# Kernel tuning notes

Hardware: AMD Instinct MI355X
Metric: run time of the kernel (lower is better)

Reference implementation:

```python
import jax, jax.numpy as jnp
import numpy as np

B, N, T, C64 = 32, 512, 24, 64


def setup_inputs() -> dict:
    key = jax.random.key(0)
    ks = jax.random.split(key, 32)
    s = 0.05
    rn = lambda k, shape: jax.random.normal(k, shape, jnp.float32) * s
    # Chebyshev polynomials of a symmetric 'scaled Laplacian' with spectral radius ~1
    rng = np.random.default_rng(0)
    A = rng.standard_normal((N, N)).astype(np.float32)
    L = (A + A.T) * (0.5 / np.sqrt(N))
    T0 = np.eye(N, dtype=np.float32)
    T1 = L
    T2 = 2.0 * (L @ L) - T0
    cheb = jnp.asarray(np.stack([T0, T1, T2]))  # (K,N,N)
    return dict(
        x=jax.random.normal(ks[0], (B, N, 1, T), jnp.float32),
        y=jax.random.normal(ks[1], (B, T, 151), jnp.float32),
        tl_w=rn(ks[2], (C64 * T, 151 * T)), tl_b=rn(ks[3], (C64 * T,)),
        u0_w=rn(ks[4], (C64 * T, T)), u0_b=rn(ks[5], (C64 * T,)),
        u1a=rn(ks[6], (N,)), u2a=rn(ks[7], (C64, N)), u3a=rn(ks[8], (C64,)),
        be_a=rn(ks[9], (1, T, T)), ve_a=rn(ks[10], (T, T)),
        u1b=rn(ks[11], (N,)), u2b=rn(ks[12], (C64, N)), u3b=rn(ks[13], (C64,)),
        be_b=rn(ks[14], (1, T, T)), ve_b=rn(ks[15], (T, T)),
        sw1=rn(ks[16], (T,)), sw2=rn(ks[17], (1, T)), sw3=rn(ks[18], (1,)),
        s_bs=rn(ks[19], (1, N, N)), s_vs=rn(ks[20], (N, N)),
        cheb=cheb, theta=rn(ks[21], (3, 1, C64)),
        l1_w=rn(ks[22], (C64 * T, C64 * T)), l1_b=rn(ks[23], (C64 * T,)),
        res_w=rn(ks[24], (C64,)), res_b=rn(ks[25], (C64,)),
        ln_g=jnp.ones((C64,), jnp.float32), ln_b=jnp.zeros((C64,), jnp.float32),
    )


def reference(x, y, tl_w, tl_b, u0_w, u0_b, u1a, u2a, u3a, be_a, ve_a,
              u1b, u2b, u3b, be_b, ve_b, sw1, sw2, sw3, s_bs, s_vs,
              cheb, theta, l1_w, l1_b, res_w, res_b, ln_g, ln_b):
    b, n, fin, t = x.shape
    # datetime embedding: Linear(151*T -> 64*T), reshaped to (B,T,64)
    dt = (y.reshape(b, -1) @ tl_w.T + tl_b).reshape(b, t, C64)

    def temporal_att(x64, u1, u2, u3, be, ve):
        # x64: (B,N,64,T); add dt broadcast over vertices
        x1 = x64 + jnp.transpose(dt, (0, 2, 1))[:, None]          # (B,N,64,T)
        lhs = jnp.einsum('bnft,n,fm->btm', x1, u1, u2)            # (B,T,N)
        rhs = jnp.einsum('f,bnft->bnt', u3, x1)                   # (B,N,T)
        prod = jnp.einsum('btn,bns->bts', lhs, rhs)               # (B,T,T)
        E = jnp.einsum('ts,bsr->btr', ve, jax.nn.sigmoid(prod + be))
        return jax.nn.softmax(E, axis=1)

    # TAt with F_in == 1: U0 (1x1 Conv1d over T channels) expands to 64 features
    xin = jnp.transpose(x.reshape(b, n, t), (0, 2, 1))            # (B,T,N)
    x0 = jnp.einsum('ot,btn->bon', u0_w, xin) + u0_b[None, :, None]  # (B,64T,N)
    x64 = jnp.transpose(x0, (0, 2, 1)).reshape(b, n, C64, t)
    E1 = temporal_att(x64, u1a, u2a, u3a, be_a, ve_a)             # (B,T,T)

    # apply temporal attention: (B,N*F,T) @ (B,T,T)
    x_tat = jnp.einsum('bnft,bts->bnfs', x, E1)                   # (B,N,1,T)

    # spatial attention
    lhs = jnp.einsum('bnft,t,fm->bnm', x_tat, sw1, sw2)           # (B,N,T)
    rhs = jnp.einsum('f,bnft->btn', sw3, x_tat)                   # (B,T,N)
    prod = jnp.einsum('bnt,btm->bnm', lhs, rhs)                   # (B,N,N)
    S = jnp.einsum('nm,bmk->bnk', s_vs, jax.nn.sigmoid(prod + s_bs))
    S = jax.nn.softmax(S, axis=1)                                 # (B,N,N)

    # K-order Chebyshev graph conv with spatial attention (vectorized over T)
    g = jnp.zeros((b, n, theta.shape[-1], t), x.dtype)
    for k in range(cheb.shape[0]):
        At = jnp.transpose(cheb[k][None] * S, (0, 2, 1))          # (B,N,N)
        tmp = jnp.einsum('bij,bjft->bift', At, x)                 # (B,N,1,T)
        g = g + jnp.einsum('bift,fo->biot', tmp, theta[k])
    g = jax.nn.relu(g)                                            # (B,N,64,T)

    # second temporal attention (F=64 path, no U0)
    E2 = temporal_att(g, u1b, u2b, u3b, be_b, ve_b)
    g2 = jnp.einsum('bnfs,bst->bnft', g, E2)                      # (B,N,64,T)

    # linear1 over flattened (64*T), then raw reshape to (B,64,N,T)
    tlin = g2.reshape(b, n, -1) @ l1_w.T + l1_b                   # (B,N,64T)
    tco = tlin.reshape(b, C64, n, t)

    # residual 1x1 conv: in_channels=1 -> 64
    res = x[:, :, 0, :][:, None] * res_w[None, :, None, None] + res_b[None, :, None, None]

    z = jax.nn.relu(res + tco)                                    # (B,64,N,T)
    z = jnp.transpose(z, (0, 3, 2, 1))                            # (B,T,N,64)
    mu = jnp.mean(z, axis=-1, keepdims=True)
    var = jnp.var(z, axis=-1, keepdims=True)
    z = (z - mu) / jnp.sqrt(var + 1e-5) * ln_g + ln_b
    return jnp.transpose(z, (0, 2, 3, 1))                         # (B,N,64,T)
```

## Files before the change

kernel.cpp:

```cpp
#include <hip/hip_runtime.h>
#include <hip/hip_bf16.h>
#include <math.h>

#define BB 32
#define NN 512
#define TT 24
#define CC 64
#define CT 1536
#define YD 3624
#define YP 3648

typedef __attribute__((ext_vector_type(4))) float f32x4;
typedef __attribute__((ext_vector_type(8))) short bf16x8;

static __device__ __forceinline__ short f2bf(float f){
  union { float f; unsigned u; } v; v.f = f;
  unsigned r = (v.u + 0x7FFF + ((v.u >> 16) & 1)) >> 16;
  return (short)r;
}
static __device__ __forceinline__ float bf2f(short s){
  union { unsigned u; float f; } v; v.u = ((unsigned)(unsigned short)s) << 16;
  return v.f;
}

__global__ void k_prep0(const float* __restrict__ u0_w, const float* __restrict__ u0_b,
                        const float* __restrict__ u1a, const float* __restrict__ u3a,
                        const float* __restrict__ u1b,
                        float* __restrict__ w0u3, float* __restrict__ b0u3, float* __restrict__ sums){
  int tid = threadIdx.x;
  if (tid < 576){
    int tp = tid / TT, t = tid % TT;
    float acc = 0.f;
    for (int f = 0; f < CC; ++f) acc += u3a[f] * u0_w[(f*TT + tp)*TT + t];
    w0u3[tid] = acc;
  }
  if (tid < TT){
    float acc = 0.f;
    for (int f = 0; f < CC; ++f) acc += u3a[f] * u0_b[f*TT + tid];
    b0u3[tid] = acc;
  }
  if (tid == 0){ float s = 0.f; for (int n = 0; n < NN; ++n) s += u1a[n]; sums[0] = s; }
  if (tid == 1){ float s = 0.f; for (int n = 0; n < NN; ++n) s += u1b[n]; sums[1] = s; }
}

__global__ __launch_bounds__(256) void k_pre(const float* __restrict__ s_vs, const float* __restrict__ y,
                    const float* __restrict__ tl_w, const float* __restrict__ cheb,
                    const float* __restrict__ x, const float* __restrict__ l1_w,
                    const float* __restrict__ s_bs,
                    __hip_bfloat16* __restrict__ svB, __hip_bfloat16* __restrict__ yB,
                    __hip_bfloat16* __restrict__ WB, short* __restrict__ chT,
                    short* __restrict__ xTb, __hip_bfloat16* __restrict__ Wb,
                    float* __restrict__ sbT){
  __shared__ float shm[512*25];
  int bb = blockIdx.x, tid = threadIdx.x;
  if (bb < 256){
    int i = (bb*256 + tid)*4;
    float4 v = *(const float4*)(s_vs + i);
    svB[i+0] = __float2bfloat16(v.x);
    svB[i+1] = __float2bfloat16(v.y);
    svB[i+2] = __float2bfloat16(v.z);
    svB[i+3] = __float2bfloat16(v.w);
  } else if (bb < 313){
    int gid = (bb - 256)*256 + tid;
    int r = gid / (YP/8), c8 = (gid % (YP/8))*8;
    if (r < 32){
      bf16x8 o;
      if (c8 < YD){
        float4 a = *(const float4*)(y + (size_t)r*YD + c8);
        float4 b = *(const float4*)(y + (size_t)r*YD + c8 + 4);
        o[0]=f2bf(a.x); o[1]=f2bf(a.y); o[2]=f2bf(a.z); o[3]=f2bf(a.w);
        o[4]=f2bf(b.x); o[5]=f2bf(b.y); o[6]=f2bf(b.z); o[7]=f2bf(b.w);
      } else {
        for (int j = 0; j < 8; ++j) o[j] = 0;
      }
      *(bf16x8*)((short*)yB + (size_t)r*YP + c8) = o;
    }
  } else if (bb < 3049){
    int gid = (bb - 313)*256 + tid;
    int r = gid / (YP/8), c8 = (gid % (YP/8))*8;
    if (r < 1536){
      bf16x8 o;
      if (c8 < YD){
        float4 a = *(const float4*)(tl_w + (size_t)r*YD + c8);
        float4 b = *(const float4*)(tl_w + (size_t)r*YD + c8 + 4);
        o[0]=f2bf(a.x); o[1]=f2bf(a.y); o[2]=f2bf(a.z); o[3]=f2bf(a.w);
        o[4]=f2bf(b.x); o[5]=f2bf(b.y); o[6]=f2bf(b.z); o[7]=f2bf(b.w);
      } else {
        for (int j = 0; j < 8; ++j) o[j] = 0;
      }
      *(bf16x8*)((short*)WB + (size_t)r*YP + c8) = o;
    }
  } else if (bb < 3817){
    int q = bb - 3049;
    int jt = q & 15, it = (q >> 4) & 15, k = q >> 8;
    float (*ts)[33] = (float(*)[33])shm;
    int c = tid & 31, r8 = tid >> 5;
    #pragma unroll
    for (int p = 0; p < 4; ++p){
      int r = p*8 + r8;
      ts[r][c] = cheb[((size_t)k*NN + jt*32 + r)*NN + it*32 + c];
    }
    __syncthreads();
    #pragma unroll
    for (int p = 0; p < 4; ++p){
      int r = p*8 + r8;
      chT[((size_t)k*NN + it*32 + r)*NN + jt*32 + c] = f2bf(ts[c][r]);
    }
  } else if (bb < 3849){
    int b = bb - 3817;
    for (int idx = tid; idx < NN*TT; idx += 256){
      int j = idx / TT, t = idx % TT;
      shm[j*25 + t] = x[(size_t)b*NN*TT + idx];
    }
    __syncthreads();
    for (int u = tid; u < 32*64; u += 256){
      int t = u >> 6, j8 = (u & 63)*8;
      bf16x8 o;
      if (t < TT){
        #pragma unroll
        for (int e = 0; e < 8; ++e) o[e] = f2bf(shm[(j8 + e)*25 + t]);
      } else {
        #pragma unroll
        for (int e = 0; e < 8; ++e) o[e] = 0;
      }
      *(bf16x8*)(xTb + ((size_t)b*32 + t)*NN + j8) = o;
    }
  } else if (bb < 6153){
    int i = ((bb - 3849)*256 + tid)*4;
    float4 v = *(const float4*)(l1_w + i);
    Wb[i+0] = __float2bfloat16(v.x);
    Wb[i+1] = __float2bfloat16(v.y);
    Wb[i+2] = __float2bfloat16(v.z);
    Wb[i+3] = __float2bfloat16(v.w);
  } else {
    int q = bb - 6153;
    int mt = q & 15, kt = q >> 4;
    float (*ts)[33] = (float(*)[33])shm;
    int c = tid & 31, r8 = tid >> 5;
    #pragma unroll
    for (int p = 0; p < 4; ++p){
      int r = p*8 + r8;
      ts[r][c] = s_bs[(size_t)(mt*32 + r)*NN + kt*32 + c];
    }
    __syncthreads();
    #pragma unroll
    for (int p = 0; p < 4; ++p){
      int r = p*8 + r8;
      sbT[(size_t)(kt*32 + r)*NN + mt*32 + c] = ts[c][r];
    }
  }
}

__global__ __launch_bounds__(256) void k_dtgemm(const __hip_bfloat16* __restrict__ yB,
                       const __hip_bfloat16* __restrict__ WB, float* __restrict__ pdt){
  __shared__ __align__(16) short lA[32*32];
  __shared__ __align__(16) short lB[256*32];
  int nt = blockIdx.x, ks = blockIdx.y;
  int o0 = nt*256;
  int tid = threadIdx.x;
  int w = tid >> 6, l = tid & 63;
  int lrow = l & 15, lk = l >> 4;
  f32x4 acc[2][4];
  #pragma unroll
  for (int m = 0; m < 2; ++m)
    #pragma unroll
    for (int n = 0; n < 4; ++n) acc[m][n] = (f32x4){0.f,0.f,0.f,0.f};
  for (int step = 0; step < 6; ++step){
    int k0 = (ks*6 + step)*32;
    #pragma unroll
    for (int p = 0; p < 4; ++p){
      int c = p*4 + w;
      int off = c*512 + l*8;
      int row = off >> 5, col = off & 31;
      __builtin_amdgcn_global_load_lds(
        (const __attribute__((address_space(1))) void*)((const short*)WB + (size_t)(o0 + row)*YP + k0 + col),
        (__attribute__((address_space(3))) void*)(lB + c*512), 16, 0, 0);
    }
    if (w < 2){
      int off = w*512 + l*8;
      int row = off >> 5, col = off & 31;
      __builtin_amdgcn_global_load_lds(
        (const __attribute__((address_space(1))) void*)((const short*)yB + (size_t)row*YP + k0 + col),
        (__attribute__((address_space(3))) void*)(lA + w*512), 16, 0, 0);
    }
    __syncthreads();
    bf16x8 a[2], bv[4];
    #pragma unroll
    for (int m = 0; m < 2; ++m) a[m] = *(const bf16x8*)(lA + (m*16 + lrow)*32 + lk*8);
    #pragma unroll
    for (int n = 0; n < 4; ++n) bv[n] = *(const bf16x8*)(lB + (w*64 + n*16 + lrow)*32 + lk*8);
    #pragma unroll
    for (int m = 0; m < 2; ++m)
      #pragma unroll
      for (int n = 0; n < 4; ++n)
        acc[m][n] = __builtin_amdgcn_mfma_f32_16x16x32_bf16(a[m], bv[n], acc[m][n], 0, 0, 0);
    __syncthreads();
  }
  #pragma unroll
  for (int m = 0; m < 2; ++m){
    #pragma unroll
    for (int n = 0; n < 4; ++n){
      int o = o0 + w*64 + n*16 + lrow;
      #pragma unroll
      for (int j = 0; j < 4; ++j){
        int b = m*16 + lk*4 + j;
        pdt[((size_t)(ks*32 + b))*CT + o] = acc[m][n][j];
      }
    }
  }
}

__global__ void k_small(const float* __restrict__ x, const float* __restrict__ pdt,
                        const float* __restrict__ tl_b,
                        const float* __restrict__ u0_w, const float* __restrict__ u0_b,
                        const float* __restrict__ u1a, const float* __restrict__ u3a,
                        const float* __restrict__ u3b, const float* __restrict__ sums,
                        float* __restrict__ dt,
                        float* __restrict__ w1a, float* __restrict__ du3a, float* __restrict__ du3b){
  __shared__ float xu_s[TT], u1a_s[NN], dt_s[CT];
  int b = blockIdx.x, tid = threadIdx.x;
  for (int o = tid; o < CT; o += 256){
    float acc = tl_b[o];
    #pragma unroll
    for (int ks = 0; ks < 19; ++ks) acc += pdt[((size_t)(ks*32 + b))*CT + o];
    dt_s[o] = acc;
    dt[b*CT + o] = acc;
  }
  for (int i = tid; i < NN; i += 256) u1a_s[i] = u1a[i];
  __syncthreads();
  int wv = tid >> 6, ln = tid & 63;
  for (int t = wv; t < TT; t += 4){
    float acc = 0.f;
    for (int n = ln; n < NN; n += 64) acc += u1a_s[n]*x[(size_t)(b*NN + n)*TT + t];
    for (int off = 32; off; off >>= 1) acc += __shfl_down(acc, off);
    if (ln == 0) xu_s[t] = acc;
  }
  if (tid < TT){
    float a = 0.f, c = 0.f;
    for (int f = 0; f < CC; ++f){
      float d = dt_s[tid*CC + f];
      a += u3a[f]*d; c += u3b[f]*d;
    }
    du3a[b*TT + tid] = a;
    du3b[b*TT + tid] = c;
  }
  __syncthreads();
  float S1 = sums[0];
  for (int idx = tid; idx < CC*TT; idx += 256){
    int f = idx / TT, tp = idx % TT;
    float acc = 0.f;
    const float* wrow = u0_w + (f*TT + tp)*TT;
    for (int t = 0; t < TT; ++t) acc += wrow[t]*xu_s[t];
    w1a[b*CC*TT + idx] = acc + S1*(u0_b[f*TT + tp] + dt_s[tp*CC + f]);
  }
}

__global__ __launch_bounds__(384) void k_rhs1(const float* __restrict__ x, const float* __restrict__ w0u3,
                      const float* __restrict__ b0u3, const float* __restrict__ du3a,
                      float* __restrict__ rhs1){
  __shared__ float xs[16*TT], w0_s[576], bd_s[TT];
  int b = blockIdx.y, n0 = blockIdx.x*16, tid = threadIdx.x;
  for (int i = tid; i < 576; i += 384) w0_s[i] = w0u3[i];
  if (tid < TT) bd_s[tid] = b0u3[tid] + du3a[b*TT + tid];
  xs[tid] = x[(size_t)(b*NN + n0)*TT + tid];
  __syncthreads();
  int nn = tid / TT, tp = tid % TT;
  float acc = bd_s[tp];
  const float* wr = w0_s + tp*TT;
  const float* xr = xs + nn*TT;
  for (int t = 0; t < TT; ++t) acc += wr[t]*xr[t];
  rhs1[(size_t)b*NN*TT + (n0 + nn)*TT + tp] = acc;
}

__global__ __launch_bounds__(576) void k_prod(const float* __restrict__ u2, const float* __restrict__ w1,
                      const float* __restrict__ rhs, float* __restrict__ pprod){
  __shared__ float u2s[64][65], w1s[CC*TT], lh[TT][64], rh[64][TT];
  int ns = blockIdx.x, b = blockIdx.y;
  int n0 = ns*64, tid = threadIdx.x;
  for (int i = tid; i < 4096; i += 576){ int f = i >> 6, n = i & 63; u2s[f][n] = u2[f*NN + n0 + n]; }
  for (int i = tid; i < CC*TT; i += 576) w1s[i] = w1[b*CC*TT + i];
  for (int i = tid; i < 1536; i += 576) ((float*)rh)[i] = rhs[(size_t)b*NN*TT + n0*TT + i];
  __syncthreads();
  for (int idx = tid; idx < 1536; idx += 576){
    int t = idx >> 6, n = idx & 63;
    float acc = 0.f;
    #pragma unroll 8
    for (int f = 0; f < CC; ++f) acc += u2s[f][n]*w1s[f*TT + t];
    lh[t][n] = acc;
  }
  __syncthreads();
  int t = tid / TT, s = tid % TT;
  float acc = 0.f;
  #pragma unroll 4
  for (int n = 0; n < 64; ++n) acc += lh[t][n]*rh[n][s];
  pprod[((size_t)(b*8 + ns))*576 + tid] = acc;
}

__global__ void k_att_post2(const float* __restrict__ pprod, const float* __restrict__ ve,
                            const float* __restrict__ be, float* __restrict__ E){
  __shared__ float sig_s[TT*TT], E_s[TT*TT];
  int b = blockIdx.x, tid = threadIdx.x;
  float acc = 0.f;
  #pragma unroll
  for (int p = 0; p < 8; ++p) acc += pprod[((size_t)(b*8 + p))*576 + tid];
  sig_s[tid] = 1.f/(1.f + expf(-(acc + be[tid])));
  __syncthreads();
  {
    int t = tid / TT, r = tid % TT;
    float a = 0.f;
    for (int s = 0; s < TT; ++s) a += ve[t*TT + s]*sig_s[s*TT + r];
    E_s[tid] = a;
  }
  __syncthreads();
  if (tid < TT){
    int r = tid;
    float mx = -1e30f;
    for (int t = 0; t < TT; ++t) mx = fmaxf(mx, E_s[t*TT + r]);
    float sum = 0.f;
    for (int t = 0; t < TT; ++t) sum += expf(E_s[t*TT + r] - mx);
    float inv = 1.f/sum;
    for (int t = 0; t < TT; ++t) E[(size_t)b*TT*TT + t*TT + r] = expf(E_s[t*TT + r] - mx)*inv;
  }
}

__global__ void k_xtat(const float* __restrict__ x, const float* __restrict__ E1,
                       const float* __restrict__ sw1, const float* __restrict__ sw2,
                       const float* __restrict__ sw3,
                       float* __restrict__ lx, float* __restrict__ r2){
  __shared__ float E_s[TT*TT], sw1_s[TT], sw2_s[TT];
  int b = blockIdx.x >> 1, half = blockIdx.x & 1, tid = threadIdx.x;
  for (int i = tid; i < 576; i += 256) E_s[i] = E1[(size_t)b*576 + i];
  if (tid < TT){ sw1_s[tid] = sw1[tid]; sw2_s[tid] = sw2[tid]; }
  __syncthreads();
  int n = half*256 + tid;
  float xr[TT];
  const float* xp = x + (size_t)(b*NN + n)*TT;
  for (int t = 0; t < TT; ++t) xr[t] = xp[t];
  float l = 0.f, r = 0.f;
  for (int s = 0; s < TT; ++s){
    float acc = 0.f;
    for (int t = 0; t < TT; ++t) acc += xr[t]*E_s[t*TT + s];
    l += acc*sw1_s[s];
    r += acc*sw2_s[s];
  }
  lx[b*NN + n] = l;
  r2[b*NN + n] = r*sw3[0];
}

__global__ __launch_bounds__(256) void k_sig(const float* __restrict__ lx, const float* __restrict__ r2,
                     const float* __restrict__ sbT, short* __restrict__ Qb){
  int b = blockIdx.y;
  int k = blockIdx.x*4 + (threadIdx.x >> 6);
  int m8 = (threadIdx.x & 63)*8;
  float r2k = r2[b*NN + k];
  const float* lxb = lx + b*NN;
  float4 l0 = *(const float4*)(lxb + m8);
  float4 l1 = *(const float4*)(lxb + m8 + 4);
  const float* sb = sbT + (size_t)k*NN + m8;
  float4 s0 = *(const float4*)(sb);
  float4 s1 = *(const float4*)(sb + 4);
  bf16x8 o;
  o[0] = f2bf(1.f/(1.f + __expf(-(l0.x*r2k + s0.x))));
  o[1] = f2bf(1.f/(1.f + __expf(-(l0.y*r2k + s0.y))));
  o[2] = f2bf(1.f/(1.f + __expf(-(l0.z*r2k + s0.z))));
  o[3] = f2bf(1.f/(1.f + __expf(-(l0.w*r2k + s0.w))));
  o[4] = f2bf(1.f/(1.f + __expf(-(l1.x*r2k + s1.x))));
  o[5] = f2bf(1.f/(1.f + __expf(-(l1.y*r2k + s1.y))));
  o[6] = f2bf(1.f/(1.f + __expf(-(l1.z*r2k + s1.z))));
  o[7] = f2bf(1.f/(1.f + __expf(-(l1.w*r2k + s1.w))));
  *(bf16x8*)(Qb + ((size_t)b*NN + k)*NN + m8) = o;
}

__global__ __launch_bounds__(256) void k_S0(const __hip_bfloat16* __restrict__ svB,
                    const short* __restrict__ Qb, float* __restrict__ ST){
  __shared__ __align__(16) short lA[128*32];
  __shared__ __align__(16) short lB[128*32];
  int kt = blockIdx.x, nt = blockIdx.y, b = blockIdx.z;
  int n0 = nt*128, k0 = kt*128;
  int tid = threadIdx.x;
  int w = tid >> 6, l = tid & 63;
  int wr = w >> 1, wc = w & 1;
  int lrow = l & 15, lk = l >> 4;
  f32x4 acc[4][4];
  #pragma unroll
  for (int m = 0; m < 4; ++m)
    #pragma unroll
    for (int n = 0; n < 4; ++n) acc[m][n] = (f32x4){0.f,0.f,0.f,0.f};
  for (int m0 = 0; m0 < NN; m0 += 32){
    #pragma unroll
    for (int p = 0; p < 2; ++p){
      int c = p*4 + w;
      int off = c*512 + l*8;
      int row = off >> 5, col = off & 31;
      __builtin_amdgcn_global_load_lds(
        (const __attribute__((address_space(1))) void*)(svB + (size_t)(n0 + row)*NN + m0 + col),
        (__attribute__((address_space(3))) void*)(lA + c*512), 16, 0, 0);
      __builtin_amdgcn_global_load_lds(
        (const __attribute__((address_space(1))) void*)(Qb + ((size_t)b*NN + k0 + row)*NN + m0 + col),
        (__attribute__((address_space(3))) void*)(lB + c*512), 16, 0, 0);
    }
    __syncthreads();
    bf16x8 a[4], bv[4];
    #pragma unroll
    for (int m = 0; m < 4; ++m) a[m] = *(const bf16x8*)(lA + (wr*64 + m*16 + lrow)*32 + lk*8);
    #pragma unroll
    for (int n = 0; n < 4; ++n) bv[n] = *(const bf16x8*)(lB + (wc*64 + n*16 + lrow)*32 + lk*8);
    #pragma unroll
    for (int m = 0; m < 4; ++m)
      #pragma unroll
      for (int n = 0; n < 4; ++n)
        acc[m][n] = __builtin_amdgcn_mfma_f32_16x16x32_bf16(a[m], bv[n], acc[m][n], 0, 0, 0);
    __syncthreads();
  }
  #pragma unroll
  for (int m = 0; m < 4; ++m){
    #pragma unroll
    for (int n = 0; n < 4; ++n){
      int col = k0 + wc*64 + n*16 + lrow;
      int row = n0 + wr*64 + m*16 + lk*4;
      float4 v; v.x = acc[m][n][0]; v.y = acc[m][n][1]; v.z = acc[m][n][2]; v.w = acc[m][n][3];
      *(float4*)(ST + (size_t)b*NN*NN + (size_t)col*NN + row) = v;
    }
  }
}

__global__ __launch_bounds__(256) void k_expS(const float* __restrict__ ST, short* __restrict__ P,
                      float* __restrict__ invZ){
  int b = blockIdx.y;
  int row = blockIdx.x*4 + (threadIdx.x >> 6);
  int l = threadIdx.x & 63;
  const float* R = ST + (size_t)b*NN*NN + (size_t)row*NN;
  float4 v0 = *(const float4*)(R + l*8);
  float4 v1 = *(const float4*)(R + l*8 + 4);
  float mx = fmaxf(fmaxf(fmaxf(v0.x,v0.y),fmaxf(v0.z,v0.w)),
                   fmaxf(fmaxf(v1.x,v1.y),fmaxf(v1.z,v1.w)));
  for (int off = 32; off; off >>= 1) mx = fmaxf(mx, __shfl_xor(mx, off));
  v0.x = __expf(v0.x-mx); v0.y = __expf(v0.y-mx); v0.z = __expf(v0.z-mx); v0.w = __expf(v0.w-mx);
  v1.x = __expf(v1.x-mx); v1.y = __expf(v1.y-mx); v1.z = __expf(v1.z-mx); v1.w = __expf(v1.w-mx);
  float s = v0.x+v0.y+v0.z+v0.w+v1.x+v1.y+v1.z+v1.w;
  for (int off = 32; off; off >>= 1) s += __shfl_xor(s, off);
  bf16x8 o;
  o[0]=f2bf(v0.x); o[1]=f2bf(v0.y); o[2]=f2bf(v0.z); o[3]=f2bf(v0.w);
  o[4]=f2bf(v1.x); o[5]=f2bf(v1.y); o[6]=f2bf(v1.z); o[7]=f2bf(v1.w);
  *(bf16x8*)(P + ((size_t)b*NN + row)*NN + l*8) = o;
  if (l == 0) invZ[b*NN + row] = 1.f/s;
}

__global__ __launch_bounds__(256) void k_tmpG(const short* __restrict__ P, const short* __restrict__ chebT,
                      const short* __restrict__ xT, const float* __restrict__ invZ,
                      float* __restrict__ tmp){
  __shared__ __align__(16) short lP[128*32];
  __shared__ __align__(16) short lC[128*32];
  __shared__ __align__(16) short lX[32*32];
  __shared__ float iz_s[128];
  int it = blockIdx.x, kc = blockIdx.y, b = blockIdx.z;
  int i0 = it*128;
  int tid = threadIdx.x;
  int w = tid >> 6, l = tid & 63;
  int lrow = l & 15, lk = l >> 4;
  if (tid < 128) iz_s[tid] = invZ[b*NN + i0 + tid];
  f32x4 acc[2][2];
  #pragma unroll
  for (int m = 0; m < 2; ++m)
    #pragma unroll
    for (int n = 0; n < 2; ++n) acc[m][n] = (f32x4){0.f,0.f,0.f,0.f};
  for (int ks = 0; ks < 16; ++ks){
    int k0 = ks*32;
    #pragma unroll
    for (int p = 0; p < 2; ++p){
      int c = p*4 + w;
      int off = c*512 + l*8;
      int row = off >> 5, col = off & 31;
      __builtin_amdgcn_global_load_lds(
        (const __attribute__((address_space(1))) void*)(P + ((size_t)b*NN + i0 + row)*NN + k0 + col),
        (__attribute__((address_space(3))) void*)(lP + c*512), 16, 0, 0);
      __builtin_amdgcn_global_load_lds(
        (const __attribute__((address_space(1))) void*)(chebT + ((size_t)kc*NN + i0 + row)*NN + k0 + col),
        (__attribute__((address_space(3))) void*)(lC + c*512), 16, 0, 0);
    }
    if (w < 2){
      int off = w*512 + l*8;
      int row = off >> 5, col = off & 31;
      __builtin_amdgcn_global_load_lds(
        (const __attribute__((address_space(1))) void*)(xT + ((size_t)b*32 + row)*NN + k0 + col),
        (__attribute__((address_space(3))) void*)(lX + w*512), 16, 0, 0);
    }
    __syncthreads();
    bf16x8 a[2], bv[2];
    #pragma unroll
    for (int m = 0; m < 2; ++m){
      int r = w*32 + m*16 + lrow;
      bf16x8 pp = *(const bf16x8*)(lP + r*32 + lk*8);
      bf16x8 cc = *(const bf16x8*)(lC + r*32 + lk*8);
      bf16x8 af;
      #pragma unroll
      for (int e = 0; e < 8; ++e) af[e] = f2bf(bf2f(pp[e])*bf2f(cc[e]));
      a[m] = af;
    }
    #pragma unroll
    for (int n = 0; n < 2; ++n) bv[n] = *(const bf16x8*)(lX + (n*16 + lrow)*32 + lk*8);
    #pragma unroll
    for (int m = 0; m < 2; ++m)
      #pragma unroll
      for (int n = 0; n < 2; ++n)
        acc[m][n] = __builtin_amdgcn_mfma_f32_16x16x32_bf16(a[m], bv[n], acc[m][n], 0, 0, 0);
    __syncthreads();
  }
  #pragma unroll
  for (int m = 0; m < 2; ++m){
    #pragma unroll
    for (int n = 0; n < 2; ++n){
      int t = n*16 + lrow;
      if (t < TT){
        #pragma unroll
        for (int j = 0; j < 4; ++j){
          int ir = w*32 + m*16 + lk*4 + j;
          tmp[((size_t)(kc*BB + b)*NN + i0 + ir)*TT + t] = acc[m][n][j]*iz_s[ir];
        }
      }
    }
  }
}

__global__ __launch_bounds__(384) void k_gsum(const float* __restrict__ tmp, const float* __restrict__ theta,
                      const float* __restrict__ u1b, const float* __restrict__ u3b,
                      const float* __restrict__ du3b,
                      float* __restrict__ rhsg, float* __restrict__ pw1g){
  __shared__ float A0[16*TT], A1[16*TT], A2[16*TT], th_s[192], u3_s[CC], u1_s[16], du_s[TT];
  int nt = blockIdx.x, b = blockIdx.y;
  int n0 = nt*16, tid = threadIdx.x;
  for (int i = tid; i < 192; i += 384) th_s[i] = theta[i];
  if (tid < CC) u3_s[tid] = u3b[tid];
  if (tid < 16) u1_s[tid] = u1b[n0 + tid];
  if (tid < TT) du_s[tid] = du3b[b*TT + tid];
  A0[tid] = tmp[((size_t)(0*BB + b)*NN + n0)*TT + tid];
  A1[tid] = tmp[((size_t)(1*BB + b)*NN + n0)*TT + tid];
  A2[tid] = tmp[((size_t)(2*BB + b)*NN + n0)*TT + tid];
  __syncthreads();
  {
    int nn = tid / TT, t = tid % TT;
    float a0 = A0[nn*TT + t], a1 = A1[nn*TT + t], a2 = A2[nn*TT + t];
    float acc = du_s[t];
    #pragma unroll 8
    for (int f = 0; f < CC; ++f){
      float v = th_s[f]*a0 + th_s[64 + f]*a1 + th_s[128 + f]*a2;
      acc += u3_s[f]*fmaxf(v, 0.f);
    }
    rhsg[(size_t)b*NN*TT + (n0 + nn)*TT + t] = acc;
  }
  #pragma unroll
  for (int p = 0; p < 4; ++p){
    int o = tid + p*384;
    int f = o / TT, t = o % TT;
    float t0 = th_s[f], t1 = th_s[64 + f], t2 = th_s[128 + f];
    float acc = 0.f;
    #pragma unroll
    for (int m = 0; m < 16; ++m){
      float v = t0*A0[m*TT + t] + t1*A1[m*TT + t] + t2*A2[m*TT + t];
      acc += u1_s[m]*fmaxf(v, 0.f);
    }
    pw1g[((size_t)(b*32 + nt))*CC*TT + o] = acc;
  }
}

__global__ void k_w1g_red(const float* __restrict__ pw1g, const float* __restrict__ dt,
                          const float* __restrict__ sums, float* __restrict__ w1g){
  int b = blockIdx.x, tid = threadIdx.x;
  float S2 = sums[1];
  for (int o = tid; o < CC*TT; o += 256){
    int f = o / TT, t = o % TT;
    float acc = 0.f;
    for (int nt = 0; nt < 32; ++nt) acc += pw1g[((size_t)(b*32 + nt))*CC*TT + o];
    w1g[b*CC*TT + o] = acc + S2*dt[b*CT + t*CC + f];
  }
}

__global__ void k_g2(const float* __restrict__ tmp, const float* __restrict__ E2,
                     const float* __restrict__ theta, __hip_bfloat16* __restrict__ g2){
  __shared__ float E_s[TT*TT], th_s[192], tr[3*4*TT], g_s[4*CT];
  int b = blockIdx.y, n0 = blockIdx.x*4, tid = threadIdx.x;
  for (int i = tid; i < 576; i += 256) E_s[i] = E2[(size_t)b*576 + i];
  for (int i = tid; i < 192; i += 256) th_s[i] = theta[i];
  for (int i = tid; i < 288; i += 256){
    int k = i / 96, rem = i % 96, nn = rem / TT, s = rem % TT;
    tr[i] = tmp[((size_t)(k*BB + b)*NN + n0 + nn)*TT + s];
  }
  __syncthreads();
  for (int idx = tid; idx < 4*CT; idx += 256){
    int nn = idx / CT, rem = idx % CT, f = rem / TT, s = rem % TT;
    float v = th_s[f]*tr[nn*TT + s] + th_s[64 + f]*tr[96 + nn*TT + s] + th_s[128 + f]*tr[192 + nn*TT + s];
    g_s[idx] = fmaxf(v, 0.f);
  }
  __syncthreads();
  for (int idx = tid; idx < 4*CT; idx += 256){
    int nn = idx / CT, rem = idx % CT, f = rem / TT, t = rem % TT;
    float acc = 0.f;
    const float* gr = g_s + nn*CT + f*TT;
    for (int s = 0; s < TT; ++s) acc += gr[s]*E_s[s*TT + t];
    g2[(size_t)(b*NN + n0 + nn)*CT + rem] = __float2bfloat16(acc);
  }
}

__global__ __launch_bounds__(256) void k_gemm_bf16(const __hip_bfloat16* __restrict__ A,
                      const __hip_bfloat16* __restrict__ W,
                      const float* __restrict__ bias, __hip_bfloat16* __restrict__ Cout){
  int bid = blockIdx.x;
  int nb = (bid & 7)*192 + (bid >> 3);
  int o0 = (nb % 12)*128, i0 = (nb / 12)*128;
  __shared__ __align__(16) short lA[128*64];
  __shared__ __align__(16) short lB[128*64];
  int tid = threadIdx.x;
  int w = tid >> 6, l = tid & 63;
  int wr = w >> 1, wc = w & 1;
  int lrow = l & 15, lk = l >> 4;
  int srow = l >> 3;
  int scol = ((l & 7) ^ srow)*8;
  int swz = (lrow & 7) << 3;
  f32x4 acc[4][4];
  #pragma unroll
  for (int m = 0; m < 4; ++m)
    #pragma unroll
    for (int n = 0; n < 4; ++n) acc[m][n] = (f32x4){0.f,0.f,0.f,0.f};
  for (int k0 = 0; k0 < CT; k0 += 64){
    #pragma unroll
    for (int p = 0; p < 4; ++p){
      int c = p*4 + w;
      __builtin_amdgcn_global_load_lds(
        (const __attribute__((address_space(1))) void*)(A + (size_t)(i0 + c*8 + srow)*CT + k0 + scol),
        (__attribute__((address_space(3))) void*)(lA + c*512), 16, 0, 0);
      __builtin_amdgcn_global_load_lds(
        (const __attribute__((address_space(1))) void*)(W + (size_t)(o0 + c*8 + srow)*CT + k0 + scol),
        (__attribute__((address_space(3))) void*)(lB + c*512), 16, 0, 0);
    }
    __syncthreads();
    #pragma unroll
    for (int h = 0; h < 2; ++h){
      bf16x8 a[4], bv[4];
      #pragma unroll
      for (int m = 0; m < 4; ++m){
        int row = wr*64 + m*16 + lrow;
        a[m] = *(const bf16x8*)(lA + row*64 + ((h*32 + lk*8) ^ swz));
      }
      #pragma unroll
      for (int n = 0; n < 4; ++n){
        int row = wc*64 + n*16 + lrow;
        bv[n] = *(const bf16x8*)(lB + row*64 + ((h*32 + lk*8) ^ swz));
      }
      #pragma unroll
      for (int m = 0; m < 4; ++m)
        #pragma unroll
        for (int n = 0; n < 4; ++n)
          acc[m][n] = __builtin_amdgcn_mfma_f32_16x16x32_bf16(a[m], bv[n], acc[m][n], 0, 0, 0);
    }
    __syncthreads();
  }
  #pragma unroll
  for (int m = 0; m < 4; ++m){
    #pragma unroll
    for (int n = 0; n < 4; ++n){
      int o = o0 + wc*64 + n*16 + lrow;
      float bo = bias[o];
      #pragma unroll
      for (int j = 0; j < 4; ++j){
        int i = i0 + wr*64 + m*16 + lk*4 + j;
        Cout[(size_t)i*CT + o] = __float2bfloat16(acc[m][n][j] + bo);
      }
    }
  }
}

__global__ __launch_bounds__(128) void k_final(const __hip_bfloat16* __restrict__ tlin, const float* __restrict__ x,
                      const float* __restrict__ res_w, const float* __restrict__ res_b,
                      const float* __restrict__ ln_g, const float* __restrict__ ln_b,
                      float* __restrict__ out){
  __shared__ float Ls[64][132];
  __shared__ float rw_s[64], rb_s[64], lg_s[64], lb_s[64];
  int ot = blockIdx.x, dlt = blockIdx.y, b = blockIdx.z;
  int o0 = ot*128, tid = threadIdx.x;
  if (tid < 64){ rw_s[tid]=res_w[tid]; rb_s[tid]=res_b[tid]; lg_s[tid]=ln_g[tid]; lb_s[tid]=ln_b[tid]; }
  const __hip_bfloat16* tb = tlin + (size_t)b*NN*CT;
  #pragma unroll 4
  for (int c = 0; c < 64; ++c)
    Ls[c][tid] = __bfloat162float(tb[(size_t)(c*8 + dlt)*CT + o0 + tid]);
  __syncthreads();
  int p = dlt*CT + o0 + tid;
  int np = p / TT, tp = p % TT;
  float xv = x[(size_t)(b*NN + np)*TT + tp];
  float z[CC];
  float sum = 0.f, sq = 0.f;
  #pragma unroll
  for (int c = 0; c < CC; ++c){
    float v = Ls[c][tid] + xv*rw_s[c] + rb_s[c];
    v = fmaxf(v, 0.f);
    z[c] = v; sum += v; sq += v*v;
  }
  float mu = sum*(1.f/64.f);
  float var = sq*(1.f/64.f) - mu*mu;
  float rstd = rsqrtf(var + 1e-5f);
  float* ob = out + (size_t)(b*NN + np)*CC*TT + tp;
  #pragma unroll
  for (int c = 0; c < CC; ++c)
    ob[c*TT] = (z[c] - mu)*rstd*lg_s[c] + lb_s[c];
}

extern "C" void kernel_launch(void* const* d_in, const int* in_sizes, int n_in,
                              void* d_out, int out_size, void* d_ws, size_t ws_size,
                              hipStream_t stream){
  const float* x    = (const float*)d_in[0];
  const float* y    = (const float*)d_in[1];
  const float* tl_w = (const float*)d_in[2];
  const float* tl_b = (const float*)d_in[3];
  const float* u0_w = (const float*)d_in[4];
  const float* u0_b = (const float*)d_in[5];
  const float* u1a  = (const float*)d_in[6];
  const float* u2a  = (const float*)d_in[7];
  const float* u3a  = (const float*)d_in[8];
  const float* be_a = (const float*)d_in[9];
  const float* ve_a = (const float*)d_in[10];
  const float* u1b  = (const float*)d_in[11];
  const float* u2b  = (const float*)d_in[12];
  const float* u3b  = (const float*)d_in[13];
  const float* be_b = (const float*)d_in[14];
  const float* ve_b = (const float*)d_in[15];
  const float* sw1  = (const float*)d_in[16];
  const float* sw2  = (const float*)d_in[17];
  const float* sw3  = (const float*)d_in[18];
  const float* s_bs = (const float*)d_in[19];
  const float* s_vs = (const float*)d_in[20];
  const float* cheb = (const float*)d_in[21];
  const float* theta= (const float*)d_in[22];
  const float* l1_w = (const float*)d_in[23];
  const float* l1_b = (const float*)d_in[24];
  const float* res_w= (const float*)d_in[25];
  const float* res_b= (const float*)d_in[26];
  const float* ln_g = (const float*)d_in[27];
  const float* ln_b = (const float*)d_in[28];
  float* out = (float*)d_out;
  float* ws  = (float*)d_ws;

  float* dt   = ws;
  float* E    = dt   + 49152;
  float* lxp  = E    + 18432;
  float* r2p  = lxp  + 16384;
  float* w0u3 = r2p  + 16384;
  float* b0u3 = w0u3 + 640;
  float* sums = b0u3 + 64;
  float* du3a = sums + 64;
  float* du3b = du3a + 768;
  float* w1a  = du3b + 768;
  float* w1g  = w1a  + 49152;
  float* lhs1 = w1g  + 49152;
  float* rhs1 = lhs1 + 393216;
  float* lhsg = rhs1 + 393216;
  float* rhsg = lhsg + 393216;
  float* svBf = rhsg + 393216;
  float* ppr  = svBf + 131072;
  float* tmp  = ppr  + 147456;
  float* big  = tmp  + 1179648;
  float* ST   = big;
  float* pw1g = big;
  __hip_bfloat16* tlin = (__hip_bfloat16*)big;
  __hip_bfloat16* WB = (__hip_bfloat16*)big;
  __hip_bfloat16* yB = (__hip_bfloat16*)(big + 2801664);
  float* pdt = big + 2801664 + 58368;
  short* Pb  = (short*)(big + 8388608);
  short* xTb = (short*)(big + 12582912);
  float* iZ  = big + 12582912 + 262144;
  short* chT = (short*)(big + 12582912 + 262144 + 16384);
  __hip_bfloat16* Wb = (__hip_bfloat16*)(big + 13254656);
  short* Qb  = (short*)(big + 14434304);
  float* sbT = big + 18628608;
  __hip_bfloat16* svB = (__hip_bfloat16*)svBf;
  __hip_bfloat16* g2b = (__hip_bfloat16*)d_out;

  k_prep0<<<dim3(1), dim3(576), 0, stream>>>(u0_w, u0_b, u1a, u3a, u1b, w0u3, b0u3, sums);
  k_pre<<<dim3(6409), dim3(256), 0, stream>>>(s_vs, y, tl_w, cheb, x, l1_w, s_bs, svB, yB, WB, chT, xTb, Wb, sbT);
  k_dtgemm<<<dim3(6, 19), dim3(256), 0, stream>>>(yB, WB, pdt);
  k_small<<<dim3(32), dim3(256), 0, stream>>>(x, pdt, tl_b, u0_w, u0_b, u1a, u3a, u3b, sums, dt, w1a, du3a, du3b);
  k_rhs1<<<dim3(32, 32), dim3(384), 0, stream>>>(x, w0u3, b0u3, du3a, rhs1);
  k_prod<<<dim3(8, 32), dim3(576), 0, stream>>>(u2a, w1a, rhs1, ppr);
  k_att_post2<<<dim3(32), dim3(576), 0, stream>>>(ppr, ve_a, be_a, E);
  k_xtat<<<dim3(64), dim3(256), 0, stream>>>(x, E, sw1, sw2, sw3, lxp, r2p);
  k_sig<<<dim3(128, 32), dim3(256), 0, stream>>>(lxp, r2p, sbT, Qb);
  k_S0<<<dim3(4, 4, 32), dim3(256), 0, stream>>>(svB, Qb, ST);
  k_expS<<<dim3(128, 32), dim3(256), 0, stream>>>(ST, Pb, iZ);
  k_tmpG<<<dim3(4, 3, 32), dim3(256), 0, stream>>>(Pb, chT, xTb, iZ, tmp);
  k_gsum<<<dim3(32, 32), dim3(384), 0, stream>>>(tmp, theta, u1b, u3b, du3b, rhsg, pw1g);
  k_w1g_red<<<dim3(32), dim3(256), 0, stream>>>(pw1g, dt, sums, w1g);
  k_prod<<<dim3(8, 32), dim3(576), 0, stream>>>(u2b, w1g, rhsg, ppr);
  k_att_post2<<<dim3(32), dim3(576), 0, stream>>>(ppr, ve_b, be_b, E);
  k_g2<<<dim3(128, 32), dim3(256), 0, stream>>>(tmp, E, theta, g2b);
  k_gemm_bf16<<<dim3(1536), dim3(256), 0, stream>>>(g2b, Wb, l1_b, tlin);
  k_final<<<dim3(12, 8, 32), dim3(128), 0, stream>>>(tlin, x, res_w, res_b, ln_g, ln_b, out);
}
```

Baseline: 403.8 us.

## Fuse small attention kernels and fold prep into preprocessing launch

Merges the tiny prep kernel into an extra block of k_pre, fuses the rhs computation into the first prod kernel, and folds the attention post-processing (sum, sigmoid, ve matmul, softmax) into k_xtat. It also widens the w1g reduction to a 2D grid with one output per thread. The goal is fewer launches and fewer small global round-trips on a launch-bound pipeline. The cost is redundant softmax work in both k_xtat blocks per batch and heavier per-block shared memory in the fused kernel.

```diff
diff --git a/kernel.cpp b/kernel.cpp
--- a/kernel.cpp
+++ b/kernel.cpp
@@ -23,34 +23,18 @@
   return v.f;
 }
 
-__global__ void k_prep0(const float* __restrict__ u0_w, const float* __restrict__ u0_b,
-                        const float* __restrict__ u1a, const float* __restrict__ u3a,
-                        const float* __restrict__ u1b,
-                        float* __restrict__ w0u3, float* __restrict__ b0u3, float* __restrict__ sums){
-  int tid = threadIdx.x;
-  if (tid < 576){
-    int tp = tid / TT, t = tid % TT;
-    float acc = 0.f;
-    for (int f = 0; f < CC; ++f) acc += u3a[f] * u0_w[(f*TT + tp)*TT + t];
-    w0u3[tid] = acc;
-  }
-  if (tid < TT){
-    float acc = 0.f;
-    for (int f = 0; f < CC; ++f) acc += u3a[f] * u0_b[f*TT + tid];
-    b0u3[tid] = acc;
-  }
-  if (tid == 0){ float s = 0.f; for (int n = 0; n < NN; ++n) s += u1a[n]; sums[0] = s; }
-  if (tid == 1){ float s = 0.f; for (int n = 0; n < NN; ++n) s += u1b[n]; sums[1] = s; }
-}
-
 __global__ __launch_bounds__(256) void k_pre(const float* __restrict__ s_vs, const float* __restrict__ y,
                     const float* __restrict__ tl_w, const float* __restrict__ cheb,
                     const float* __restrict__ x, const float* __restrict__ l1_w,
                     const float* __restrict__ s_bs,
+                    const float* __restrict__ u0_w, const float* __restrict__ u0_b,
+                    const float* __restrict__ u1a, const float* __restrict__ u3a,
+                    const float* __restrict__ u1b,
                     __hip_bfloat16* __restrict__ svB, __hip_bfloat16* __restrict__ yB,
                     __hip_bfloat16* __restrict__ WB, short* __restrict__ chT,
                     short* __restrict__ xTb, __hip_bfloat16* __restrict__ Wb,
-                    float* __restrict__ sbT){
+                    float* __restrict__ sbT,
+                    float* __restrict__ w0u3, float* __restrict__ b0u3, float* __restrict__ sums){
   __shared__ float shm[512*25];
   int bb = blockIdx.x, tid = threadIdx.x;
   if (bb < 256){
@@ -132,7 +116,7 @@
     Wb[i+1] = __float2bfloat16(v.y);
     Wb[i+2] = __float2bfloat16(v.z);
     Wb[i+3] = __float2bfloat16(v.w);
-  } else {
+  } else if (bb < 6409){
     int q = bb - 6153;
     int mt = q & 15, kt = q >> 4;
     float (*ts)[33] = (float(*)[33])shm;
@@ -148,6 +132,21 @@
       int r = p*8 + r8;
       sbT[(size_t)(kt*32 + r)*NN + mt*32 + c] = ts[c][r];
     }
+  } else {
+    for (int e = tid; e < 576; e += 256){
+      int tp = e / TT, t = e % TT;
+      float acc = 0.f;
+      for (int f = 0; f < CC; ++f) acc += u3a[f]*u0_w[(f*TT + tp)*TT + t];
+      w0u3[e] = acc;
+    }
+    if (tid >= 64 && tid < 64 + TT){
+      int t = tid - 64;
+      float acc = 0.f;
+      for (int f = 0; f < CC; ++f) acc += u3a[f]*u0_b[f*TT + t];
+      b0u3[t] = acc;
+    }
+    if (tid == 0){ float s = 0.f; for (int n = 0; n < NN; ++n) s += u1a[n]; sums[0] = s; }
+    if (tid == 1){ float s = 0.f; for (int n = 0; n < NN; ++n) s += u1b[n]; sums[1] = s; }
   }
 }
 
@@ -255,21 +254,41 @@
   }
 }
 
-__global__ __launch_bounds__(384) void k_rhs1(const float* __restrict__ x, const float* __restrict__ w0u3,
+__global__ __launch_bounds__(576) void k_prodA(const float* __restrict__ x, const float* __restrict__ w0u3,
                       const float* __restrict__ b0u3, const float* __restrict__ du3a,
-                      float* __restrict__ rhs1){
-  __shared__ float xs[16*TT], w0_s[576], bd_s[TT];
-  int b = blockIdx.y, n0 = blockIdx.x*16, tid = threadIdx.x;
-  for (int i = tid; i < 576; i += 384) w0_s[i] = w0u3[i];
+                      const float* __restrict__ u2, const float* __restrict__ w1,
+                      float* __restrict__ pprod){
+  __shared__ float u2s[64][65], w1s[CC*TT], lh[TT][64], rh[64][TT], xs[64*TT], w0_s[576], bd_s[TT];
+  int ns = blockIdx.x, b = blockIdx.y;
+  int n0 = ns*64, tid = threadIdx.x;
+  for (int i = tid; i < 4096; i += 576){ int f = i >> 6, n = i & 63; u2s[f][n] = u2[f*NN + n0 + n]; }
+  for (int i = tid; i < CC*TT; i += 576) w1s[i] = w1[b*CC*TT + i];
+  for (int i = tid; i < 1536; i += 576) xs[i] = x[(size_t)(b*NN + n0)*TT + i];
+  w0_s[tid] = w0u3[tid];
   if (tid < TT) bd_s[tid] = b0u3[tid] + du3a[b*TT + tid];
-  xs[tid] = x[(size_t)(b*NN + n0)*TT + tid];
-  __syncthreads();
-  int nn = tid / TT, tp = tid % TT;
-  float acc = bd_s[tp];
-  const float* wr = w0_s + tp*TT;
-  const float* xr = xs + nn*TT;
-  for (int t = 0; t < TT; ++t) acc += wr[t]*xr[t];
-  rhs1[(size_t)b*NN*TT + (n0 + nn)*TT + tp] = acc;
+  __syncthreads();
+  for (int idx = tid; idx < 1536; idx += 576){
+    int n = idx / TT, tp = idx % TT;
+    float acc = bd_s[tp];
+    const float* wr = w0_s + tp*TT;
+    const float* xr = xs + n*TT;
+    #pragma unroll
+    for (int t = 0; t < TT; ++t) acc += wr[t]*xr[t];
+    rh[n][tp] = acc;
+  }
+  for (int idx = tid; idx < 1536; idx += 576){
+    int t = idx >> 6, n = idx & 63;
+    float acc = 0.f;
+    #pragma unroll 8
+    for (int f = 0; f < CC; ++f) acc += u2s[f][n]*w1s[f*TT + t];
+    lh[t][n] = acc;
+  }
+  __syncthreads();
+  int t = tid / TT, s = tid % TT;
+  float acc = 0.f;
+  #pragma unroll 4
+  for (int n = 0; n < 64; ++n) acc += lh[t][n]*rh[n][s];
+  pprod[((size_t)(b*8 + ns))*576 + tid] = acc;
 }
 
 __global__ __launch_bounds__(576) void k_prod(const float* __restrict__ u2, const float* __restrict__ w1,
@@ -323,14 +342,37 @@
   }
 }
 
-__global__ void k_xtat(const float* __restrict__ x, const float* __restrict__ E1,
+__global__ __launch_bounds__(256) void k_xtat(const float* __restrict__ ppr, const float* __restrict__ ve,
+                       const float* __restrict__ be, const float* __restrict__ x,
                        const float* __restrict__ sw1, const float* __restrict__ sw2,
                        const float* __restrict__ sw3,
                        float* __restrict__ lx, float* __restrict__ r2){
-  __shared__ float E_s[TT*TT], sw1_s[TT], sw2_s[TT];
+  __shared__ float sig_s[576], E_s[576], sw1_s[TT], sw2_s[TT];
   int b = blockIdx.x >> 1, half = blockIdx.x & 1, tid = threadIdx.x;
-  for (int i = tid; i < 576; i += 256) E_s[i] = E1[(size_t)b*576 + i];
+  for (int i = tid; i < 576; i += 256){
+    float acc = 0.f;
+    #pragma unroll
+    for (int p = 0; p < 8; ++p) acc += ppr[((size_t)(b*8 + p))*576 + i];
+    sig_s[i] = 1.f/(1.f + expf(-(acc + be[i])));
+  }
   if (tid < TT){ sw1_s[tid] = sw1[tid]; sw2_s[tid] = sw2[tid]; }
+  __syncthreads();
+  for (int i = tid; i < 576; i += 256){
+    int t = i / TT, r = i % TT;
+    float a = 0.f;
+    for (int s = 0; s < TT; ++s) a += ve[t*TT + s]*sig_s[s*TT + r];
+    E_s[i] = a;
+  }
+  __syncthreads();
+  if (tid < TT){
+    int r = tid;
+    float mx = -1e30f;
+    for (int t = 0; t < TT; ++t) mx = fmaxf(mx, E_s[t*TT + r]);
+    float sum = 0.f;
+    for (int t = 0; t < TT; ++t) sum += expf(E_s[t*TT + r] - mx);
+    float inv = 1.f/sum;
+    for (int t = 0; t < TT; ++t) E_s[t*TT + r] = expf(E_s[t*TT + r] - mx)*inv;
+  }
   __syncthreads();
   int n = half*256 + tid;
   float xr[TT];
@@ -563,16 +605,16 @@
   }
 }
 
-__global__ void k_w1g_red(const float* __restrict__ pw1g, const float* __restrict__ dt,
+__global__ __launch_bounds__(128) void k_w1g_red(const float* __restrict__ pw1g, const float* __restrict__ dt,
                           const float* __restrict__ sums, float* __restrict__ w1g){
-  int b = blockIdx.x, tid = threadIdx.x;
+  int b = blockIdx.y;
+  int o = blockIdx.x*128 + threadIdx.x;
+  int f = o / TT, t = o % TT;
   float S2 = sums[1];
-  for (int o = tid; o < CC*TT; o += 256){
-    int f = o / TT, t = o % TT;
-    float acc = 0.f;
-    for (int nt = 0; nt < 32; ++nt) acc += pw1g[((size_t)(b*32 + nt))*CC*TT + o];
-    w1g[b*CC*TT + o] = acc + S2*dt[b*CT + t*CC + f];
-  }
+  float acc = 0.f;
+  #pragma unroll 8
+  for (int nt = 0; nt < 32; ++nt) acc += pw1g[((size_t)(b*32 + nt))*CC*TT + o];
+  w1g[b*CC*TT + o] = acc + S2*dt[b*CT + t*CC + f];
 }
 
 __global__ void k_g2(const float* __restrict__ tmp, const float* __restrict__ E2,
@@ -773,20 +815,20 @@
   __hip_bfloat16* svB = (__hip_bfloat16*)svBf;
   __hip_bfloat16* g2b = (__hip_bfloat16*)d_out;
 
-  k_prep0<<<dim3(1), dim3(576), 0, stream>>>(u0_w, u0_b, u1a, u3a, u1b, w0u3, b0u3, sums);
-  k_pre<<<dim3(6409), dim3(256), 0, stream>>>(s_vs, y, tl_w, cheb, x, l1_w, s_bs, svB, yB, WB, chT, xTb, Wb, sbT);
+  k_pre<<<dim3(6410), dim3(256), 0, stream>>>(s_vs, y, tl_w, cheb, x, l1_w, s_bs,
+                                              u0_w, u0_b, u1a, u3a, u1b,
+                                              svB, yB, WB, chT, xTb, Wb, sbT,
+                                              w0u3, b0u3, sums);
   k_dtgemm<<<dim3(6, 19), dim3(256), 0, stream>>>(yB, WB, pdt);
   k_small<<<dim3(32), dim3(256), 0, stream>>>(x, pdt, tl_b, u0_w, u0_b, u1a, u3a, u3b, sums, dt, w1a, du3a, du3b);
-  k_rhs1<<<dim3(32, 32), dim3(384), 0, stream>>>(x, w0u3, b0u3, du3a, rhs1);
-  k_prod<<<dim3(8, 32), dim3(576), 0, stream>>>(u2a, w1a, rhs1, ppr);
-  k_att_post2<<<dim3(32), dim3(576), 0, stream>>>(ppr, ve_a, be_a, E);
-  k_xtat<<<dim3(64), dim3(256), 0, stream>>>(x, E, sw1, sw2, sw3, lxp, r2p);
+  k_prodA<<<dim3(8, 32), dim3(576), 0, stream>>>(x, w0u3, b0u3, du3a, u2a, w1a, ppr);
+  k_xtat<<<dim3(64), dim3(256), 0, stream>>>(ppr, ve_a, be_a, x, sw1, sw2, sw3, lxp, r2p);
   k_sig<<<dim3(128, 32), dim3(256), 0, stream>>>(lxp, r2p, sbT, Qb);
   k_S0<<<dim3(4, 4, 32), dim3(256), 0, stream>>>(svB, Qb, ST);
   k_expS<<<dim3(128, 32), dim3(256), 0, stream>>>(ST, Pb, iZ);
   k_tmpG<<<dim3(4, 3, 32), dim3(256), 0, stream>>>(Pb, chT, xTb, iZ, tmp);
   k_gsum<<<dim3(32, 32), dim3(384), 0, stream>>>(tmp, theta, u1b, u3b, du3b, rhsg, pw1g);
-  k_w1g_red<<<dim3(32), dim3(256), 0, stream>>>(pw1g, dt, sums, w1g);
+  k_w1g_red<<<dim3(12, 32), dim3(128), 0, stream>>>(pw1g, dt, sums, w1g);
   k_prod<<<dim3(8, 32), dim3(576), 0, stream>>>(u2b, w1g, rhsg, ppr);
   k_att_post2<<<dim3(32), dim3(576), 0, stream>>>(ppr, ve_b, be_b, E);
   k_g2<<<dim3(128, 32), dim3(256), 0, stream>>>(tmp, E, theta, g2b);
```

After: 382.8 us. 5.2% less time.
